# Kernel tuning notes

Hardware: AMD Instinct MI355X
Metric: run time of the kernel (lower is better)

Reference implementation:

```python
import jax, jax.numpy as jnp
import numpy as np

B, T, E, V = 128, 64, 300, 50000
C, HI, WI = 512, 14, 14
HID, K, L = 1024, 512, 2


def setup_inputs() -> dict:
    key = jax.random.key(0)
    ks = jax.random.split(key, 16)
    s = 0.05
    return {
        "desc": jax.random.randint(ks[0], (B, T), 0, V),
        "img": jax.random.normal(ks[1], (B, C, HI, WI), jnp.float32),
        "emb": jax.random.normal(ks[2], (V, E), jnp.float32) * 0.1,
        "W_ih": jax.random.normal(ks[3], (4 * HID, E), jnp.float32) * s,
        "W_hh": jax.random.normal(ks[4], (4 * HID, HID), jnp.float32) * s,
        "b_ih": jnp.zeros((4 * HID,), jnp.float32),
        "b_hh": jnp.zeros((4 * HID,), jnp.float32),
        "W_img": jax.random.normal(ks[5], (HID, C), jnp.float32) * s,
        "b_img": jnp.zeros((HID,), jnp.float32),
        "Wl_img": jax.random.normal(ks[6], (L, K, HID), jnp.float32) * s,
        "Wl_q": jax.random.normal(ks[7], (L, K, HID), jnp.float32) * s,
        "bl_q": jnp.zeros((L, K), jnp.float32),
        "wl_p": jax.random.normal(ks[8], (L, K), jnp.float32) * s,
        "bl_p": jnp.zeros((L,), jnp.float32),
    }


def _lstm_last(x, W_ih, W_hh, b_ih, b_hh):
    # x: [T, B, E]; returns last-step hidden state h_T: [B, HID]
    hid = W_hh.shape[1]
    h0 = jnp.zeros((x.shape[1], hid), x.dtype)

    def step(carry, xt):
        h, c = carry
        g = xt @ W_ih.T + b_ih + h @ W_hh.T + b_hh
        i, f, gg, o = jnp.split(g, 4, axis=-1)  # torch gate order i,f,g,o
        c = jax.nn.sigmoid(f) * c + jax.nn.sigmoid(i) * jnp.tanh(gg)
        h = jax.nn.sigmoid(o) * jnp.tanh(c)
        return (h, c), None

    (h, _), _ = jax.lax.scan(step, (h0, h0), x)
    return h


def reference(desc, img, emb, W_ih, W_hh, b_ih, b_hh, W_img, b_img,
              Wl_img, Wl_q, bl_q, wl_p, bl_p):
    # --- text branch ---
    e = emb[desc]                       # [B, T, E] embedding gather
    x = e.reshape(T, B, E)              # faithful: torch uses reshape, NOT transpose
    u_k = _lstm_last(x, W_ih, W_hh, b_ih, b_hh)  # [B, HID]

    # --- image branch ---
    n_areas = HI * WI
    img_r = img.reshape(B, n_areas, C)  # faithful: reshape, NOT permute
    out_img = img_r @ W_img.T + b_img   # [B, N, HID]

    # --- stacked additive attention ---
    for i in range(L):
        t_img = out_img @ Wl_img[i].T                      # [B, N, K]
        t_u = u_k @ Wl_q[i].T + bl_q[i]                    # [B, K]
        h_a = jnp.tanh(t_img + t_u[:, None, :])            # [B, N, K]
        p = jax.nn.softmax(h_a @ wl_p[i] + bl_p[i], axis=1)  # [B, N]
        temp = out_img.reshape(B, HID, n_areas)            # faithful reshape
        v = jnp.einsum("bhn,bn->bh", temp, p)              # [B, HID]
        u_k = v + u_k
    return u_k
```

## Files before the change

### kernel.cpp

```cpp
#include <hip/hip_runtime.h>
#include <hip/hip_bf16.h>

#define B_    128
#define T_    64
#define E_    300
#define HID_  1024
#define G4_   4096
#define C_    512
#define NA_   196
#define KATT_ 512
#define MIMG_ 25088

typedef short s16x8 __attribute__((ext_vector_type(8)));
typedef float f32x4 __attribute__((ext_vector_type(4)));

__device__ __forceinline__ unsigned short f2bf(float f) {
  __hip_bfloat16 h = __float2bfloat16(f);
  return __builtin_bit_cast(unsigned short, h);
}
__device__ __forceinline__ float bf2f(unsigned short u) {
  __hip_bfloat16 h = __builtin_bit_cast(__hip_bfloat16, u);
  return __bfloat162float(h);
}

__global__ __launch_bounds__(256) void conv_bf16(const float* __restrict__ in,
                                                 unsigned short* __restrict__ out,
                                                 int n) {
  int i = blockIdx.x * 256 + threadIdx.x;
  if (i < n) out[i] = f2bf(in[i]);
}

__global__ __launch_bounds__(256) void conv_pad320(const float* __restrict__ in,
                                                   unsigned short* __restrict__ out,
                                                   int rows) {
  int i = blockIdx.x * 256 + threadIdx.x;
  if (i >= rows * 320) return;
  int r = i / 320, k = i - r * 320;
  out[i] = (k < 300) ? f2bf(in[(size_t)r * 300 + k]) : (unsigned short)0;
}

__global__ __launch_bounds__(256) void gather_emb(const int* __restrict__ desc,
                                                  const float* __restrict__ emb,
                                                  unsigned short* __restrict__ out) {
  int i = blockIdx.x * 256 + threadIdx.x;
  int m = i / 320, k = i - m * 320;
  float v = (k < 300) ? emb[(size_t)desc[m] * 300 + k] : 0.f;
  out[i] = f2bf(v);
}

__global__ __launch_bounds__(256) void conv_whh(const float* __restrict__ in,
                                                unsigned short* __restrict__ out) {
  int o = blockIdx.x * 256 + threadIdx.x;
  int e = o & 7, lq = (o >> 3) & 63, kc = (o >> 9) & 31, seg = o >> 14;
  int nl = lq & 15, quad = lq >> 4;
  int jb = seg >> 1, nt = seg & 1;
  int r = nt * 16 + nl;
  int wrow = (r & 3) * 1024 + jb * 8 + (r >> 2);
  out[o] = f2bf(in[(size_t)wrow * 1024 + kc * 32 + quad * 8 + e]);
}

__global__ __launch_bounds__(256) void gemm_mfma(
    const unsigned short* __restrict__ A, int lda,
    const unsigned short* __restrict__ Bw, int Kd,
    const float* __restrict__ bias, const float* __restrict__ bias2,
    float* __restrict__ Cf, unsigned short* __restrict__ Cb, int ldc,
    int mode, const float* __restrict__ tu, const float* __restrict__ wp,
    float* __restrict__ sc)
{
  __shared__ unsigned short As[128 * 40];
  __shared__ unsigned short Bs[128 * 40];
  const int tid = threadIdx.x;
  const int m0 = blockIdx.y << 7, n0 = blockIdx.x << 7;
  const int w = tid >> 6, l = tid & 63;
  const int wr = w >> 1, wc = w & 1;
  const int lrow = l & 15, lk = (l >> 4) << 3;
  const int srow = tid >> 2, schunk = (tid & 3) << 3;

  f32x4 acc[4][4];
#pragma unroll
  for (int i = 0; i < 4; i++)
#pragma unroll
    for (int j = 0; j < 4; j++) acc[i][j] = (f32x4){0.f, 0.f, 0.f, 0.f};

  const unsigned short* Ap = A + (size_t)(m0 + srow) * lda + schunk;
  const unsigned short* Bp = Bw + (size_t)(n0 + srow) * Kd + schunk;
  const size_t arep = (size_t)64 * lda, brep = (size_t)64 * Kd;

  for (int k0 = 0; k0 < Kd; k0 += 32) {
    *(uint4*)&As[srow * 40 + schunk]        = *(const uint4*)(Ap + k0);
    *(uint4*)&As[(srow + 64) * 40 + schunk] = *(const uint4*)(Ap + arep + k0);
    *(uint4*)&Bs[srow * 40 + schunk]        = *(const uint4*)(Bp + k0);
    *(uint4*)&Bs[(srow + 64) * 40 + schunk] = *(const uint4*)(Bp + brep + k0);
    __syncthreads();
    s16x8 af[4], bfr[4];
#pragma unroll
    for (int i = 0; i < 4; i++) {
      af[i]  = *(const s16x8*)&As[(wr * 64 + i * 16 + lrow) * 40 + lk];
      bfr[i] = *(const s16x8*)&Bs[(wc * 64 + i * 16 + lrow) * 40 + lk];
    }
#pragma unroll
    for (int i = 0; i < 4; i++)
#pragma unroll
      for (int j = 0; j < 4; j++)
        acc[i][j] = __builtin_amdgcn_mfma_f32_16x16x32_bf16(af[i], bfr[j], acc[i][j], 0, 0, 0);
    __syncthreads();
  }

  const int quad = l >> 4;
  if (mode == 3) {
#pragma unroll
    for (int i = 0; i < 4; i++) {
#pragma unroll
      for (int r = 0; r < 4; r++) {
        int row = m0 + wr * 64 + i * 16 + quad * 4 + r;
        int b = row / NA_;
        float partial = 0.f;
#pragma unroll
        for (int j = 0; j < 4; j++) {
          int col = n0 + wc * 64 + j * 16 + lrow;
          float v = acc[i][j][r] + tu[(size_t)b * KATT_ + col];
          partial += tanhf(v) * wp[col];
        }
        partial += __shfl_xor(partial, 1);
        partial += __shfl_xor(partial, 2);
        partial += __shfl_xor(partial, 4);
        partial += __shfl_xor(partial, 8);
        if (lrow == 0) unsafeAtomicAdd(&sc[row], partial);
      }
    }
    return;
  }

#pragma unroll
  for (int i = 0; i < 4; i++) {
    int rbase = m0 + wr * 64 + i * 16 + quad * 4;
#pragma unroll
    for (int j = 0; j < 4; j++) {
      int col = n0 + wc * 64 + j * 16 + lrow;
      float badd = (bias ? bias[col] : 0.f) + (bias2 ? bias2[col] : 0.f);
      if (mode == 2) {
        ushort4 pk;
        pk.x = f2bf(acc[i][j][0] + badd);
        pk.y = f2bf(acc[i][j][1] + badd);
        pk.z = f2bf(acc[i][j][2] + badd);
        pk.w = f2bf(acc[i][j][3] + badd);
        size_t off = ((size_t)(rbase >> 7)) * 524288 + (size_t)col * 128 + (rbase & 127);
        *(ushort4*)&Cb[off] = pk;
      } else {
#pragma unroll
        for (int r = 0; r < 4; r++) {
          float v = acc[i][j][r] + badd;
          int m = rbase + r;
          if (mode == 0) Cf[(size_t)m * ldc + col] = v;
          else           Cb[(size_t)m * ldc + col] = f2bf(v);
        }
      }
    }
  }
}

__global__ __launch_bounds__(512) void lstm_step3(
    const unsigned short* __restrict__ hin,
    const unsigned short* __restrict__ Xg_t,
    const unsigned short* __restrict__ Whp,
    float* __restrict__ cbuf,
    unsigned short* __restrict__ hout,
    float* __restrict__ u,
    unsigned short* __restrict__ ub)
{
  const int tid = threadIdx.x;
  const int w = tid >> 6, l = tid & 63;
  const int mb = blockIdx.x & 1, jb = blockIdx.x >> 1;
  const int mt = w & 3, nt = w >> 2;
  const int quad = l >> 4, nl = l & 15;
  const int g = l & 3, jjl = (l >> 2) & 3;

  const int brow_a = mb * 64 + mt * 16 + nl;
  const int bq = mb * 64 + mt * 16 + quad * 4;
  const int j = jb * 8 + nt * 4 + jjl;
  const int col = (g << 10) + j;

  ushort4 xg4 = *(const ushort4*)(Xg_t + (size_t)col * 128 + bq);
  float4 c4 = *(const float4*)(cbuf + (size_t)j * 128 + bq);

  const unsigned short* Ap = hin + (size_t)brow_a * 1024 + (quad << 3);
  const unsigned short* Bp = Whp + (((size_t)(jb * 2 + nt)) << 14) + (l << 3);

  f32x4 acc0 = {0.f,0.f,0.f,0.f}, acc1 = {0.f,0.f,0.f,0.f};
#pragma unroll
  for (int kc = 0; kc < 32; kc++) {
    s16x8 a = *(const s16x8*)(Ap + (kc << 5));
    s16x8 b = *(const s16x8*)(Bp + (kc << 9));
    if (kc & 1) acc1 = __builtin_amdgcn_mfma_f32_16x16x32_bf16(a, b, acc1, 0, 0, 0);
    else        acc0 = __builtin_amdgcn_mfma_f32_16x16x32_bf16(a, b, acc0, 0, 0, 0);
  }
  f32x4 acc = acc0 + acc1;

  float cn4[4], hn4[4];
#pragma unroll
  for (int r = 0; r < 4; r++) {
    unsigned short xr = (r == 0) ? xg4.x : (r == 1) ? xg4.y : (r == 2) ? xg4.z : xg4.w;
    float v = acc[r] + bf2f(xr);
    float x1 = __shfl_xor(v, 1);
    float x2 = __shfl_xor(v, 2);
    float x3 = __shfl_xor(x1, 2);
    float gi = (g == 0) ? v  : (g == 1) ? x1 : (g == 2) ? x2 : x3;
    float gf = (g == 0) ? x1 : (g == 1) ? v  : (g == 2) ? x3 : x2;
    float gg = (g == 0) ? x2 : (g == 1) ? x3 : (g == 2) ? v  : x1;
    float go = (g == 0) ? x3 : (g == 1) ? x2 : (g == 2) ? x1 : v;
    float si = 1.f / (1.f + expf(-gi));
    float sf = 1.f / (1.f + expf(-gf));
    float so = 1.f / (1.f + expf(-go));
    float cprev = (r == 0) ? c4.x : (r == 1) ? c4.y : (r == 2) ? c4.z : c4.w;
    float cn = sf * cprev + si * tanhf(gg);
    cn4[r] = cn;
    hn4[r] = so * tanhf(cn);
  }
  if (g == 0) {
    float4 co = {cn4[0], cn4[1], cn4[2], cn4[3]};
    *(float4*)(cbuf + (size_t)j * 128 + bq) = co;
#pragma unroll
    for (int r = 0; r < 4; r++)
      hout[(size_t)(bq + r) * 1024 + j] = f2bf(hn4[r]);
    if (u) {
#pragma unroll
      for (int r = 0; r < 4; r++) {
        size_t idx = (size_t)(bq + r) * 1024 + j;
        u[idx] = hn4[r];
        ub[idx] = f2bf(hn4[r]);
      }
    }
  }
}

__global__ __launch_bounds__(512) void tu_gemm(
    const unsigned short* __restrict__ ub, const unsigned short* __restrict__ Wq,
    const float* __restrict__ bq, float* __restrict__ tu)
{
  __shared__ unsigned short Bs[16 * 1032];
  const int tid = threadIdx.x;
  const int w = tid >> 6, l = tid & 63;
  const int n0 = blockIdx.x << 4;
  const int quad = l >> 4, nl = l & 15;
  for (int i = tid; i < 2048; i += 512) {
    int r = i >> 7, ch = i & 127;
    *(uint4*)&Bs[r * 1032 + ch * 8] = *(const uint4*)(Wq + (size_t)(n0 + r) * 1024 + ch * 8);
  }
  __syncthreads();
  const unsigned short* Ap = ub + (size_t)(w * 16 + nl) * 1024;
  f32x4 acc0 = {0.f,0.f,0.f,0.f}, acc1 = {0.f,0.f,0.f,0.f};
#pragma unroll 8
  for (int kc = 0; kc < 32; kc++) {
    s16x8 a = *(const s16x8*)(Ap + (kc << 5) + (quad << 3));
    s16x8 b = *(const s16x8*)&Bs[nl * 1032 + (kc << 5) + (quad << 3)];
    if (kc & 1) acc1 = __builtin_amdgcn_mfma_f32_16x16x32_bf16(a, b, acc1, 0, 0, 0);
    else        acc0 = __builtin_amdgcn_mfma_f32_16x16x32_bf16(a, b, acc0, 0, 0, 0);
  }
  f32x4 acc = acc0 + acc1;
  int colg = n0 + nl;
  float badd = bq[colg];
#pragma unroll
  for (int r = 0; r < 4; r++)
    tu[(size_t)(w * 16 + quad * 4 + r) * KATT_ + colg] = acc[r] + badd;
}

__global__ __launch_bounds__(256) void softmax_pool2(
    const float* __restrict__ sc, const unsigned short* __restrict__ outimg,
    float* __restrict__ u)
{
  int hg = blockIdx.x, b = blockIdx.y, tid = threadIdx.x;
  __shared__ float p[NA_];
  __shared__ float red[8];
  float v = (tid < NA_) ? sc[b * NA_ + tid] : -1e30f;
  float m = v;
#pragma unroll
  for (int off = 32; off; off >>= 1) m = fmaxf(m, __shfl_down(m, off, 64));
  if ((tid & 63) == 0) red[tid >> 6] = m;
  __syncthreads();
  float bm = fmaxf(fmaxf(red[0], red[1]), fmaxf(red[2], red[3]));
  float e = (tid < NA_) ? expf(v - bm) : 0.f;
  float s = e;
#pragma unroll
  for (int off = 32; off; off >>= 1) s += __shfl_down(s, off, 64);
  if ((tid & 63) == 0) red[4 + (tid >> 6)] = s;
  __syncthreads();
  float bs = red[4] + red[5] + red[6] + red[7];
  if (tid < NA_) p[tid] = e / bs;
  __syncthreads();
  int h = hg * 128 + (tid >> 1);
  int half = tid & 1;
  const unsigned short* r = outimg + (size_t)b * (HID_ * NA_) + (size_t)h * NA_ + half * 98;
  float acc = 0.f;
#pragma unroll 7
  for (int n = 0; n < 98; n += 2) {
    unsigned int pk = *(const unsigned int*)(r + n);
    acc += bf2f((unsigned short)(pk & 0xffff)) * p[half * 98 + n];
    acc += bf2f((unsigned short)(pk >> 16))    * p[half * 98 + n + 1];
  }
  acc += __shfl_xor(acc, 1);
  if (half == 0) u[(size_t)b * HID_ + h] += acc;
}

extern "C" void kernel_launch(void* const* d_in, const int* in_sizes, int n_in,
                              void* d_out, int out_size, void* d_ws, size_t ws_size,
                              hipStream_t stream) {
  const int*   desc   = (const int*)  d_in[0];
  const float* img    = (const float*)d_in[1];
  const float* emb    = (const float*)d_in[2];
  const float* W_ih   = (const float*)d_in[3];
  const float* W_hh   = (const float*)d_in[4];
  const float* b_ih   = (const float*)d_in[5];
  const float* b_hh   = (const float*)d_in[6];
  const float* W_img  = (const float*)d_in[7];
  const float* b_img  = (const float*)d_in[8];
  const float* Wl_img = (const float*)d_in[9];
  const float* Wl_q   = (const float*)d_in[10];
  const float* bl_q   = (const float*)d_in[11];
  const float* wl_p   = (const float*)d_in[12];
  float* u = (float*)d_out;

  uint8_t* base = (uint8_t*)d_ws;
  unsigned short* Xgb    = (unsigned short*)(base);
  unsigned short* imgb   = (unsigned short*)(base);
  unsigned short* outimg = (unsigned short*)(base + 67108864);
  unsigned short* Whp    = (unsigned short*)(base + 118489088);
  unsigned short* Wihb   = (unsigned short*)(base + 126877696);
  unsigned short* Aemb   = (unsigned short*)(base + 129499136);
  unsigned short* Wimgb  = (unsigned short*)(base + 134742016);
  unsigned short* Wlimgb = (unsigned short*)(base + 135790592);
  unsigned short* Wlqb   = (unsigned short*)(base + 137887744);
  unsigned short* ubb    = (unsigned short*)(base + 139984896);
  unsigned short* h0b    = (unsigned short*)(base + 140247040);
  unsigned short* h1b    = (unsigned short*)(base + 140509184);
  float*          tub    = (float*)(base + 140771328);
  float*          scb0   = (float*)(base + 141033472);
  float*          scb1   = (float*)(base + 141133824);
  float*          cbuf   = (float*)(base + 141234176);

  conv_whh<<<16384, 256, 0, stream>>>(W_hh, Whp);
  conv_pad320<<<(G4_ * 320 + 255) / 256, 256, 0, stream>>>(W_ih, Wihb, G4_);
  gather_emb<<<(8192 * 320) / 256, 256, 0, stream>>>(desc, emb, Aemb);
  conv_bf16<<<(HID_ * C_ + 255) / 256, 256, 0, stream>>>(W_img, Wimgb, HID_ * C_);
  conv_bf16<<<(2 * KATT_ * HID_ + 255) / 256, 256, 0, stream>>>(Wl_img, Wlimgb, 2 * KATT_ * HID_);
  conv_bf16<<<(2 * KATT_ * HID_ + 255) / 256, 256, 0, stream>>>(Wl_q, Wlqb, 2 * KATT_ * HID_);

  hipMemsetAsync(h0b, 0, 262144, stream);
  hipMemsetAsync(cbuf, 0, 524288, stream);
  hipMemsetAsync(scb0, 0, 200704, stream);

  gemm_mfma<<<dim3(32, 64), 256, 0, stream>>>(Aemb, 320, Wihb, 320, b_ih, b_hh,
                                              nullptr, Xgb, 0, 2, nullptr, nullptr, nullptr);

  for (int t = 0; t < T_; t++) {
    const unsigned short* hi = (t & 1) ? h1b : h0b;
    unsigned short* ho = (t & 1) ? h0b : h1b;
    lstm_step3<<<256, 512, 0, stream>>>(hi, Xgb + (size_t)t * 524288, Whp, cbuf, ho,
                                        (t == T_ - 1) ? u : nullptr,
                                        (t == T_ - 1) ? ubb : nullptr);
  }

  conv_bf16<<<(MIMG_ * C_ + 255) / 256, 256, 0, stream>>>(img, imgb, MIMG_ * C_);
  gemm_mfma<<<dim3(8, 196), 256, 0, stream>>>(imgb, C_, Wimgb, C_, b_img, nullptr,
                                              nullptr, outimg, HID_, 1, nullptr, nullptr, nullptr);

  for (int i = 0; i < 2; i++) {
    float* scb = (i == 0) ? scb0 : scb1;
    if (i == 1)
      conv_bf16<<<512, 256, 0, stream>>>(u, ubb, B_ * HID_);
    tu_gemm<<<32, 512, 0, stream>>>(ubb, Wlqb + (size_t)i * KATT_ * HID_,
                                    bl_q + i * KATT_, tub);
    gemm_mfma<<<dim3(4, 196), 256, 0, stream>>>(outimg, HID_,
                                                Wlimgb + (size_t)i * KATT_ * HID_, HID_,
                                                nullptr, nullptr, nullptr, nullptr, 0, 3,
                                                tub, wl_p + i * KATT_, scb);
    softmax_pool2<<<dim3(8, B_), 256, 0, stream>>>(scb, outimg, u);
  }
}
```

Baseline: 1.377 ms.

## Fuse all LSTM timesteps into one persistent kernel with grid barrier

Replaces the 64 per-timestep LSTM kernel launches with a single persistent kernel. It keeps the W_hh fragments in registers and the cell state in registers, stages h in swizzled LDS, and synchronises blocks each step through a global atomic counter barrier. This removes launch overhead and the repeated reload of W_hh and c per step. It relies on all 256 blocks being co-resident, and a spin barrier could deadlock if they are not. The GEMM kernel also gains an inner loop over N tiles, so each block handles 4 column tiles with fewer blocks, which reduces parallelism in those GEMMs.

```diff
diff --git a/kernel.cpp b/kernel.cpp
--- a/kernel.cpp
+++ b/kernel.cpp
@@ -13,6 +13,7 @@
 
 typedef short s16x8 __attribute__((ext_vector_type(8)));
 typedef float f32x4 __attribute__((ext_vector_type(4)));
+typedef unsigned long long u64;
 
 __device__ __forceinline__ unsigned short f2bf(float f) {
   __hip_bfloat16 h = __float2bfloat16(f);
@@ -65,109 +66,114 @@
     const float* __restrict__ bias, const float* __restrict__ bias2,
     float* __restrict__ Cf, unsigned short* __restrict__ Cb, int ldc,
     int mode, const float* __restrict__ tu, const float* __restrict__ wp,
-    float* __restrict__ sc)
+    float* __restrict__ sc, int nloop)
 {
   __shared__ unsigned short As[128 * 40];
   __shared__ unsigned short Bs[128 * 40];
   const int tid = threadIdx.x;
-  const int m0 = blockIdx.y << 7, n0 = blockIdx.x << 7;
+  const int m0 = blockIdx.y << 7;
   const int w = tid >> 6, l = tid & 63;
   const int wr = w >> 1, wc = w & 1;
   const int lrow = l & 15, lk = (l >> 4) << 3;
   const int srow = tid >> 2, schunk = (tid & 3) << 3;
-
-  f32x4 acc[4][4];
-#pragma unroll
-  for (int i = 0; i < 4; i++)
-#pragma unroll
-    for (int j = 0; j < 4; j++) acc[i][j] = (f32x4){0.f, 0.f, 0.f, 0.f};
+  const int quad = l >> 4;
 
   const unsigned short* Ap = A + (size_t)(m0 + srow) * lda + schunk;
-  const unsigned short* Bp = Bw + (size_t)(n0 + srow) * Kd + schunk;
   const size_t arep = (size_t)64 * lda, brep = (size_t)64 * Kd;
 
-  for (int k0 = 0; k0 < Kd; k0 += 32) {
-    *(uint4*)&As[srow * 40 + schunk]        = *(const uint4*)(Ap + k0);
-    *(uint4*)&As[(srow + 64) * 40 + schunk] = *(const uint4*)(Ap + arep + k0);
-    *(uint4*)&Bs[srow * 40 + schunk]        = *(const uint4*)(Bp + k0);
-    *(uint4*)&Bs[(srow + 64) * 40 + schunk] = *(const uint4*)(Bp + brep + k0);
-    __syncthreads();
-    s16x8 af[4], bfr[4];
-#pragma unroll
-    for (int i = 0; i < 4; i++) {
-      af[i]  = *(const s16x8*)&As[(wr * 64 + i * 16 + lrow) * 40 + lk];
-      bfr[i] = *(const s16x8*)&Bs[(wc * 64 + i * 16 + lrow) * 40 + lk];
-    }
+  for (int nb = 0; nb < nloop; nb++) {
+    const int n0 = (blockIdx.x * nloop + nb) << 7;
+    const unsigned short* Bp = Bw + (size_t)(n0 + srow) * Kd + schunk;
+
+    f32x4 acc[4][4];
 #pragma unroll
     for (int i = 0; i < 4; i++)
 #pragma unroll
-      for (int j = 0; j < 4; j++)
-        acc[i][j] = __builtin_amdgcn_mfma_f32_16x16x32_bf16(af[i], bfr[j], acc[i][j], 0, 0, 0);
-    __syncthreads();
-  }
-
-  const int quad = l >> 4;
-  if (mode == 3) {
-#pragma unroll
-    for (int i = 0; i < 4; i++) {
-#pragma unroll
-      for (int r = 0; r < 4; r++) {
-        int row = m0 + wr * 64 + i * 16 + quad * 4 + r;
-        int b = row / NA_;
-        float partial = 0.f;
+      for (int j = 0; j < 4; j++) acc[i][j] = (f32x4){0.f, 0.f, 0.f, 0.f};
+
+    for (int k0 = 0; k0 < Kd; k0 += 32) {
+      *(uint4*)&As[srow * 40 + schunk]        = *(const uint4*)(Ap + k0);
+      *(uint4*)&As[(srow + 64) * 40 + schunk] = *(const uint4*)(Ap + arep + k0);
+      *(uint4*)&Bs[srow * 40 + schunk]        = *(const uint4*)(Bp + k0);
+      *(uint4*)&Bs[(srow + 64) * 40 + schunk] = *(const uint4*)(Bp + brep + k0);
+      __syncthreads();
+      s16x8 af[4], bfr[4];
+#pragma unroll
+      for (int i = 0; i < 4; i++) {
+        af[i]  = *(const s16x8*)&As[(wr * 64 + i * 16 + lrow) * 40 + lk];
+        bfr[i] = *(const s16x8*)&Bs[(wc * 64 + i * 16 + lrow) * 40 + lk];
+      }
+#pragma unroll
+      for (int i = 0; i < 4; i++)
+#pragma unroll
+        for (int j = 0; j < 4; j++)
+          acc[i][j] = __builtin_amdgcn_mfma_f32_16x16x32_bf16(af[i], bfr[j], acc[i][j], 0, 0, 0);
+      __syncthreads();
+    }
+
+    if (mode == 3) {
+#pragma unroll
+      for (int i = 0; i < 4; i++) {
+#pragma unroll
+        for (int r = 0; r < 4; r++) {
+          int row = m0 + wr * 64 + i * 16 + quad * 4 + r;
+          int b = row / NA_;
+          float partial = 0.f;
+#pragma unroll
+          for (int j = 0; j < 4; j++) {
+            int col = n0 + wc * 64 + j * 16 + lrow;
+            float v = acc[i][j][r] + tu[(size_t)b * KATT_ + col];
+            partial += tanhf(v) * wp[col];
+          }
+          partial += __shfl_xor(partial, 1);
+          partial += __shfl_xor(partial, 2);
+          partial += __shfl_xor(partial, 4);
+          partial += __shfl_xor(partial, 8);
+          if (lrow == 0) unsafeAtomicAdd(&sc[row], partial);
+        }
+      }
+    } else {
+#pragma unroll
+      for (int i = 0; i < 4; i++) {
+        int rbase = m0 + wr * 64 + i * 16 + quad * 4;
 #pragma unroll
         for (int j = 0; j < 4; j++) {
           int col = n0 + wc * 64 + j * 16 + lrow;
-          float v = acc[i][j][r] + tu[(size_t)b * KATT_ + col];
-          partial += tanhf(v) * wp[col];
+          float badd = (bias ? bias[col] : 0.f) + (bias2 ? bias2[col] : 0.f);
+          if (mode == 2) {
+            ushort4 pk;
+            pk.x = f2bf(acc[i][j][0] + badd);
+            pk.y = f2bf(acc[i][j][1] + badd);
+            pk.z = f2bf(acc[i][j][2] + badd);
+            pk.w = f2bf(acc[i][j][3] + badd);
+            size_t off = ((size_t)(rbase >> 7)) * 524288 + (size_t)col * 128 + (rbase & 127);
+            *(ushort4*)&Cb[off] = pk;
+          } else {
+#pragma unroll
+            for (int r = 0; r < 4; r++) {
+              float v = acc[i][j][r] + badd;
+              int m = rbase + r;
+              if (mode == 0) Cf[(size_t)m * ldc + col] = v;
+              else           Cb[(size_t)m * ldc + col] = f2bf(v);
+            }
+          }
         }
-        partial += __shfl_xor(partial, 1);
-        partial += __shfl_xor(partial, 2);
-        partial += __shfl_xor(partial, 4);
-        partial += __shfl_xor(partial, 8);
-        if (lrow == 0) unsafeAtomicAdd(&sc[row], partial);
-      }
-    }
-    return;
-  }
-
-#pragma unroll
-  for (int i = 0; i < 4; i++) {
-    int rbase = m0 + wr * 64 + i * 16 + quad * 4;
-#pragma unroll
-    for (int j = 0; j < 4; j++) {
-      int col = n0 + wc * 64 + j * 16 + lrow;
-      float badd = (bias ? bias[col] : 0.f) + (bias2 ? bias2[col] : 0.f);
-      if (mode == 2) {
-        ushort4 pk;
-        pk.x = f2bf(acc[i][j][0] + badd);
-        pk.y = f2bf(acc[i][j][1] + badd);
-        pk.z = f2bf(acc[i][j][2] + badd);
-        pk.w = f2bf(acc[i][j][3] + badd);
-        size_t off = ((size_t)(rbase >> 7)) * 524288 + (size_t)col * 128 + (rbase & 127);
-        *(ushort4*)&Cb[off] = pk;
-      } else {
-#pragma unroll
-        for (int r = 0; r < 4; r++) {
-          float v = acc[i][j][r] + badd;
-          int m = rbase + r;
-          if (mode == 0) Cf[(size_t)m * ldc + col] = v;
-          else           Cb[(size_t)m * ldc + col] = f2bf(v);
-        }
-      }
-    }
-  }
-}
-
-__global__ __launch_bounds__(512) void lstm_step3(
-    const unsigned short* __restrict__ hin,
-    const unsigned short* __restrict__ Xg_t,
+      }
+    }
+  }
+}
+
+__global__ __launch_bounds__(512, 2) void lstm_allsteps(
+    const unsigned short* __restrict__ Xg,
     const unsigned short* __restrict__ Whp,
-    float* __restrict__ cbuf,
-    unsigned short* __restrict__ hout,
+    u64* __restrict__ hA,
+    u64* __restrict__ hB,
     float* __restrict__ u,
-    unsigned short* __restrict__ ub)
+    unsigned short* __restrict__ ub,
+    unsigned int* __restrict__ cnt)
 {
+  __shared__ unsigned short hs[64 * 1024];
+  __shared__ unsigned short louts[64 * 8];
   const int tid = threadIdx.x;
   const int w = tid >> 6, l = tid & 63;
   const int mb = blockIdx.x & 1, jb = blockIdx.x >> 1;
@@ -175,60 +181,100 @@
   const int quad = l >> 4, nl = l & 15;
   const int g = l & 3, jjl = (l >> 2) & 3;
 
-  const int brow_a = mb * 64 + mt * 16 + nl;
   const int bq = mb * 64 + mt * 16 + quad * 4;
   const int j = jb * 8 + nt * 4 + jjl;
   const int col = (g << 10) + j;
-
-  ushort4 xg4 = *(const ushort4*)(Xg_t + (size_t)col * 128 + bq);
-  float4 c4 = *(const float4*)(cbuf + (size_t)j * 128 + bq);
-
-  const unsigned short* Ap = hin + (size_t)brow_a * 1024 + (quad << 3);
-  const unsigned short* Bp = Whp + (((size_t)(jb * 2 + nt)) << 14) + (l << 3);
-
-  f32x4 acc0 = {0.f,0.f,0.f,0.f}, acc1 = {0.f,0.f,0.f,0.f};
-#pragma unroll
-  for (int kc = 0; kc < 32; kc++) {
-    s16x8 a = *(const s16x8*)(Ap + (kc << 5));
-    s16x8 b = *(const s16x8*)(Bp + (kc << 9));
-    if (kc & 1) acc1 = __builtin_amdgcn_mfma_f32_16x16x32_bf16(a, b, acc1, 0, 0, 0);
-    else        acc0 = __builtin_amdgcn_mfma_f32_16x16x32_bf16(a, b, acc0, 0, 0, 0);
-  }
-  f32x4 acc = acc0 + acc1;
-
-  float cn4[4], hn4[4];
-#pragma unroll
-  for (int r = 0; r < 4; r++) {
-    unsigned short xr = (r == 0) ? xg4.x : (r == 1) ? xg4.y : (r == 2) ? xg4.z : xg4.w;
-    float v = acc[r] + bf2f(xr);
-    float x1 = __shfl_xor(v, 1);
-    float x2 = __shfl_xor(v, 2);
-    float x3 = __shfl_xor(x1, 2);
-    float gi = (g == 0) ? v  : (g == 1) ? x1 : (g == 2) ? x2 : x3;
-    float gf = (g == 0) ? x1 : (g == 1) ? v  : (g == 2) ? x3 : x2;
-    float gg = (g == 0) ? x2 : (g == 1) ? x3 : (g == 2) ? v  : x1;
-    float go = (g == 0) ? x3 : (g == 1) ? x2 : (g == 2) ? x1 : v;
-    float si = 1.f / (1.f + expf(-gi));
-    float sf = 1.f / (1.f + expf(-gf));
-    float so = 1.f / (1.f + expf(-go));
-    float cprev = (r == 0) ? c4.x : (r == 1) ? c4.y : (r == 2) ? c4.z : c4.w;
-    float cn = sf * cprev + si * tanhf(gg);
-    cn4[r] = cn;
-    hn4[r] = so * tanhf(cn);
-  }
-  if (g == 0) {
-    float4 co = {cn4[0], cn4[1], cn4[2], cn4[3]};
-    *(float4*)(cbuf + (size_t)j * 128 + bq) = co;
-#pragma unroll
-    for (int r = 0; r < 4; r++)
-      hout[(size_t)(bq + r) * 1024 + j] = f2bf(hn4[r]);
-    if (u) {
-#pragma unroll
-      for (int r = 0; r < 4; r++) {
-        size_t idx = (size_t)(bq + r) * 1024 + j;
-        u[idx] = hn4[r];
-        ub[idx] = f2bf(hn4[r]);
-      }
+  const int arow = mt * 16 + nl;
+
+  s16x8 bfr[32];
+  {
+    const unsigned short* Bp = Whp + (((size_t)(jb * 2 + nt)) << 14) + (l << 3);
+#pragma unroll
+    for (int kc = 0; kc < 32; kc++) bfr[kc] = *(const s16x8*)(Bp + (kc << 9));
+  }
+
+  float cr[4] = {0.f, 0.f, 0.f, 0.f};
+
+  for (int step = 0; step < 64; step++) {
+    const u64* hsrc = (step & 1) ? hB : hA;
+    u64* hdst = (step & 1) ? hA : hB;
+
+    ushort4 xg4 = *(const ushort4*)(Xg + (size_t)step * 524288 + (size_t)col * 128 + bq);
+
+#pragma unroll
+    for (int it = 0; it < 16; it++) {
+      int idx = tid + (it << 9);
+      int row = idx >> 7, slot = idx & 127;
+      size_t go = (((size_t)(mb * 64 + row)) << 8) + (slot << 1);
+      u64 q0 = __hip_atomic_load(hsrc + go,     __ATOMIC_RELAXED, __HIP_MEMORY_SCOPE_AGENT);
+      u64 q1 = __hip_atomic_load(hsrc + go + 1, __ATOMIC_RELAXED, __HIP_MEMORY_SCOPE_AGENT);
+      u64* dst = (u64*)&hs[(row << 10) + ((slot ^ (row & 7)) << 3)];
+      dst[0] = q0; dst[1] = q1;
+    }
+    __syncthreads();
+
+    f32x4 acc0 = {0.f,0.f,0.f,0.f}, acc1 = {0.f,0.f,0.f,0.f};
+#pragma unroll
+    for (int kc = 0; kc < 32; kc++) {
+      int slot = ((kc << 2) | quad) ^ (arow & 7);
+      s16x8 a = *(const s16x8*)&hs[(arow << 10) + (slot << 3)];
+      if (kc & 1) acc1 = __builtin_amdgcn_mfma_f32_16x16x32_bf16(a, bfr[kc], acc1, 0, 0, 0);
+      else        acc0 = __builtin_amdgcn_mfma_f32_16x16x32_bf16(a, bfr[kc], acc0, 0, 0, 0);
+    }
+    f32x4 acc = acc0 + acc1;
+
+    float hn4[4];
+#pragma unroll
+    for (int r = 0; r < 4; r++) {
+      unsigned short xr = (r == 0) ? xg4.x : (r == 1) ? xg4.y : (r == 2) ? xg4.z : xg4.w;
+      float v = acc[r] + bf2f(xr);
+      float x1 = __shfl_xor(v, 1);
+      float x2 = __shfl_xor(v, 2);
+      float x3 = __shfl_xor(x1, 2);
+      float gi = (g == 0) ? v  : (g == 1) ? x1 : (g == 2) ? x2 : x3;
+      float gf = (g == 0) ? x1 : (g == 1) ? v  : (g == 2) ? x3 : x2;
+      float gg = (g == 0) ? x2 : (g == 1) ? x3 : (g == 2) ? v  : x1;
+      float go = (g == 0) ? x3 : (g == 1) ? x2 : (g == 2) ? x1 : v;
+      float si = 1.f / (1.f + expf(-gi));
+      float sf = 1.f / (1.f + expf(-gf));
+      float so = 1.f / (1.f + expf(-go));
+      float cn = sf * cr[r] + si * tanhf(gg);
+      cr[r] = cn;
+      hn4[r] = so * tanhf(cn);
+    }
+
+    if (step == 63) {
+      if (g == 0) {
+#pragma unroll
+        for (int r = 0; r < 4; r++) {
+          size_t idx = (size_t)(bq + r) * 1024 + j;
+          u[idx] = hn4[r];
+          ub[idx] = f2bf(hn4[r]);
+        }
+      }
+    } else {
+      if (g == 0) {
+        int rloc = mt * 16 + quad * 4;
+        int jc = nt * 4 + jjl;
+#pragma unroll
+        for (int r = 0; r < 4; r++)
+          louts[(rloc + r) * 8 + jc] = f2bf(hn4[r]);
+      }
+      __syncthreads();
+      if (tid < 128) {
+        int row = tid >> 1, half = tid & 1;
+        u64 word = *(const u64*)&louts[(row << 3) + (half << 2)];
+        size_t gi2 = (((size_t)(mb * 64 + row)) << 8) + (jb << 1) + half;
+        (void)__hip_atomic_exchange(hdst + gi2, word, __ATOMIC_RELAXED, __HIP_MEMORY_SCOPE_AGENT);
+      }
+      asm volatile("s_waitcnt vmcnt(0)" ::: "memory");
+      if (tid == 0) {
+        __hip_atomic_fetch_add(cnt, 1u, __ATOMIC_RELAXED, __HIP_MEMORY_SCOPE_AGENT);
+        unsigned int target = 256u * (unsigned)(step + 1);
+        while (__hip_atomic_load(cnt, __ATOMIC_RELAXED, __HIP_MEMORY_SCOPE_AGENT) < target)
+          __builtin_amdgcn_s_sleep(8);
+      }
+      __syncthreads();
     }
   }
 }
@@ -330,12 +376,12 @@
   unsigned short* Wlimgb = (unsigned short*)(base + 135790592);
   unsigned short* Wlqb   = (unsigned short*)(base + 137887744);
   unsigned short* ubb    = (unsigned short*)(base + 139984896);
-  unsigned short* h0b    = (unsigned short*)(base + 140247040);
-  unsigned short* h1b    = (unsigned short*)(base + 140509184);
+  u64*            hA     = (u64*)(base + 140247040);
+  u64*            hB     = (u64*)(base + 140509184);
   float*          tub    = (float*)(base + 140771328);
   float*          scb0   = (float*)(base + 141033472);
   float*          scb1   = (float*)(base + 141133824);
-  float*          cbuf   = (float*)(base + 141234176);
+  unsigned int*   cnt    = (unsigned int*)(base + 141234176);
 
   conv_whh<<<16384, 256, 0, stream>>>(W_hh, Whp);
   conv_pad320<<<(G4_ * 320 + 255) / 256, 256, 0, stream>>>(W_ih, Wihb, G4_);
@@ -344,24 +390,20 @@
   conv_bf16<<<(2 * KATT_ * HID_ + 255) / 256, 256, 0, stream>>>(Wl_img, Wlimgb, 2 * KATT_ * HID_);
   conv_bf16<<<(2 * KATT_ * HID_ + 255) / 256, 256, 0, stream>>>(Wl_q, Wlqb, 2 * KATT_ * HID_);
 
-  hipMemsetAsync(h0b, 0, 262144, stream);
-  hipMemsetAsync(cbuf, 0, 524288, stream);
+  hipMemsetAsync(hA, 0, 262144, stream);
+  hipMemsetAsync(cnt, 0, 256, stream);
   hipMemsetAsync(scb0, 0, 200704, stream);
 
-  gemm_mfma<<<dim3(32, 64), 256, 0, stream>>>(Aemb, 320, Wihb, 320, b_ih, b_hh,
-                                              nullptr, Xgb, 0, 2, nullptr, nullptr, nullptr);
-
-  for (int t = 0; t < T_; t++) {
-    const unsigned short* hi = (t & 1) ? h1b : h0b;
-    unsigned short* ho = (t & 1) ? h0b : h1b;
-    lstm_step3<<<256, 512, 0, stream>>>(hi, Xgb + (size_t)t * 524288, Whp, cbuf, ho,
-                                        (t == T_ - 1) ? u : nullptr,
-                                        (t == T_ - 1) ? ubb : nullptr);
-  }
+  gemm_mfma<<<dim3(8, 64), 256, 0, stream>>>(Aemb, 320, Wihb, 320, b_ih, b_hh,
+                                             nullptr, Xgb, 0, 2, nullptr, nullptr,
+                                             nullptr, 4);
+
+  lstm_allsteps<<<256, 512, 0, stream>>>(Xgb, Whp, hA, hB, u, ubb, cnt);
 
   conv_bf16<<<(MIMG_ * C_ + 255) / 256, 256, 0, stream>>>(img, imgb, MIMG_ * C_);
-  gemm_mfma<<<dim3(8, 196), 256, 0, stream>>>(imgb, C_, Wimgb, C_, b_img, nullptr,
-                                              nullptr, outimg, HID_, 1, nullptr, nullptr, nullptr);
+  gemm_mfma<<<dim3(2, 196), 256, 0, stream>>>(imgb, C_, Wimgb, C_, b_img, nullptr,
+                                              nullptr, outimg, HID_, 1, nullptr, nullptr,
+                                              nullptr, 4);
 
   for (int i = 0; i < 2; i++) {
     float* scb = (i == 0) ? scb0 : scb1;
@@ -369,10 +411,10 @@
       conv_bf16<<<512, 256, 0, stream>>>(u, ubb, B_ * HID_);
     tu_gemm<<<32, 512, 0, stream>>>(ubb, Wlqb + (size_t)i * KATT_ * HID_,
                                     bl_q + i * KATT_, tub);
-    gemm_mfma<<<dim3(4, 196), 256, 0, stream>>>(outimg, HID_,
+    gemm_mfma<<<dim3(1, 196), 256, 0, stream>>>(outimg, HID_,
                                                 Wlimgb + (size_t)i * KATT_ * HID_, HID_,
                                                 nullptr, nullptr, nullptr, nullptr, 0, 3,
-                                                tub, wl_p + i * KATT_, scb);
+                                                tub, wl_p + i * KATT_, scb, 4);
     softmax_pool2<<<dim3(8, B_), 256, 0, stream>>>(scb, outimg, u);
   }
 }
```

New measurement: 1.457 ms. 1.06x slower.
